# Kernel optimization log

Hardware: AMD Instinct MI355X
Metric: run time of the kernel (lower is better)

## Reference

```python
import jax, jax.numpy as jnp
import numpy as np

N_NODES, N_EDGES, D_IN, D_OUT = 50000, 800000, 64, 64
N_REL, N_TIME = 500, 1000


def setup_inputs() -> dict:
    key = jax.random.key(0)
    ks = jax.random.split(key, 14)
    xavier = lambda k, shape: jax.random.normal(k, shape, jnp.float32) * np.sqrt(2.0 / (shape[0] + shape[1])) * np.sqrt(2.0)
    return {
        "x": jax.random.normal(ks[0], (N_NODES, D_IN), jnp.float32),
        "rel_repr": jax.random.normal(ks[1], (N_REL, D_IN), jnp.float32),
        "time_emds": jax.random.normal(ks[2], (N_TIME, D_IN), jnp.float32),
        "src": jax.random.randint(ks[3], (N_EDGES,), 0, N_NODES),
        "dst": jax.random.randint(ks[4], (N_EDGES,), 0, N_NODES),
        "etype": jax.random.randint(ks[5], (N_EDGES,), 0, N_REL),
        "etime": jax.random.randint(ks[6], (N_EDGES,), 0, N_TIME),
        "trans_w": xavier(ks[7], (D_IN, D_OUT)),
        "loop_w": xavier(ks[8], (D_IN, D_OUT)),
        "w_rel": xavier(ks[9], (D_IN, D_OUT)),
        "attn_h": xavier(ks[10], (D_IN, 1)),
        "attn_t": xavier(ks[11], (D_IN, 1)),
        "attn_r": xavier(ks[12], (D_IN, 1)),
        "attn_ts": xavier(ks[13], (D_IN, 1)),
    }


def reference(x, rel_repr, time_emds, src, dst, etype, etime,
              trans_w, loop_w, w_rel, attn_h, attn_t, attn_r, attn_ts):
    n = x.shape[0]
    # per-node / per-rel / per-time scalar attention projections
    h_att = (x @ attn_h)[:, 0]          # [N]
    t_att = (x @ attn_t)[:, 0]          # [N]
    r_att = (rel_repr @ attn_r)[:, 0]   # [R]
    ts_att = (time_emds @ attn_ts)[:, 0]  # [T]
    # edge attention logits + edge_softmax grouped by destination node
    e = jax.nn.leaky_relu(h_att[src] - t_att[dst] + r_att[etype] + ts_att[etime], 0.1)  # [E]
    m = jax.ops.segment_max(e, dst, num_segments=n)
    ex = jnp.exp(e - m[dst])
    den = jax.ops.segment_sum(ex, dst, num_segments=n)
    att = (ex / den[dst])[:, None]      # [E,1]
    # message: (head + time) * (rel + time) -> trans_w -> weighted scatter-sum to dst
    time_emd = time_emds[etime]         # [E,D]
    edge_data = (x[src] + time_emd) * (rel_repr[etype] + time_emd)
    msg = (edge_data @ trans_w) * att   # [E,D_out]
    h = jax.ops.segment_sum(msg, dst, num_segments=n)
    x_out = h + x @ loop_w
    rel_out = rel_repr @ w_rel
    return (x_out, rel_out)
```

## Files before the change

kernel.cpp:

```cpp
#include <hip/hip_runtime.h>
#include <hip/hip_bf16.h>

#define N_NODES 50000
#define N_EDGES 800000
#define D 64
#define N_REL 500
#define N_TIME 1000
#define SLOTS 64
#define NODE_BLOCKS ((N_NODES + 63) / 64)
#define REL_BLOCKS  ((N_REL + 63) / 64)

__device__ __forceinline__ float bf2f(unsigned short u) {
    union { unsigned int i; float f; } v;
    v.i = ((unsigned int)u) << 16;
    return v.f;
}

__global__ void proj_kernel(const float* __restrict__ x,
                            const float* __restrict__ rel,
                            const float* __restrict__ tim,
                            const float* __restrict__ ah,
                            const float* __restrict__ at,
                            const float* __restrict__ ar,
                            const float* __restrict__ ats,
                            float* __restrict__ h_att, float* __restrict__ t_att,
                            float* __restrict__ r_att, float* __restrict__ ts_att,
                            unsigned short* __restrict__ x_bf) {
    int wave = (blockIdx.x * blockDim.x + threadIdx.x) >> 6;
    int lane = threadIdx.x & 63;
    const int total = N_NODES + N_REL + N_TIME;
    if (wave >= total) return;
    if (wave < N_NODES) {
        float xv = x[wave * D + lane];
        __hip_bfloat16 b = __float2bfloat16(xv);
        x_bf[wave * D + lane] = *(unsigned short*)&b;
        float s1 = xv * ah[lane];
        float s2 = xv * at[lane];
        for (int off = 32; off; off >>= 1) {
            s1 += __shfl_down(s1, off);
            s2 += __shfl_down(s2, off);
        }
        if (lane == 0) { h_att[wave] = s1; t_att[wave] = s2; }
    } else if (wave < N_NODES + N_REL) {
        int r = wave - N_NODES;
        float v = rel[r * D + lane] * ar[lane];
        for (int off = 32; off; off >>= 1) v += __shfl_down(v, off);
        if (lane == 0) r_att[r] = v;
    } else {
        int t = wave - N_NODES - N_REL;
        float v = tim[t * D + lane] * ats[lane];
        for (int off = 32; off; off >>= 1) v += __shfl_down(v, off);
        if (lane == 0) ts_att[t] = v;
    }
}

__global__ void build_kernel(const int* __restrict__ src, const int* __restrict__ dst,
                             const int* __restrict__ etype, const int* __restrict__ etime,
                             const float* __restrict__ h_att, const float* __restrict__ t_att,
                             const float* __restrict__ r_att, const float* __restrict__ ts_att,
                             int* __restrict__ cnt, int2* __restrict__ payload) {
    int i = blockIdx.x * blockDim.x + threadIdx.x;
    int e0 = i * 4;
    if (e0 >= N_EDGES) return;
    int4 s4 = *(const int4*)(src + e0);
    int4 d4 = *(const int4*)(dst + e0);
    int4 r4 = *(const int4*)(etype + e0);
    int4 t4 = *(const int4*)(etime + e0);
    int ss[4] = {s4.x, s4.y, s4.z, s4.w};
    int dd[4] = {d4.x, d4.y, d4.z, d4.w};
    int rr[4] = {r4.x, r4.y, r4.z, r4.w};
    int tt[4] = {t4.x, t4.y, t4.z, t4.w};
#pragma unroll
    for (int j = 0; j < 4; j++) {
        int s = ss[j], d = dd[j], r = rr[j], t = tt[j];
        float lg = h_att[s] - t_att[d] + r_att[r] + ts_att[t];
        float lr = lg > 0.f ? lg : 0.1f * lg;
        float ex = __expf(lr);
        unsigned exb = __float_as_uint(ex);
        int2 pl;
        pl.x = (int)((exb & ~7u) | (unsigned)(s & 7));
        pl.y = (int)(((unsigned)(s >> 3) << 19) | ((unsigned)r << 10) | (unsigned)t);
        int pos = atomicAdd(&cnt[d], 1);
        if (pos < SLOTS) payload[(d << 6) + pos] = pl;
    }
}

__global__ void node_gather_kernel(const unsigned short* __restrict__ x_bf,
                                   const float* __restrict__ rel,
                                   const float* __restrict__ tim,
                                   const int* __restrict__ cnt,
                                   const int2* __restrict__ payload,
                                   float* __restrict__ agg) {
    int d = (blockIdx.x * blockDim.x + threadIdx.x) >> 6;
    int lane = threadIdx.x & 63;
    if (d >= N_NODES) return;
    int deg = cnt[d];
    if (deg > SLOTS) deg = SLOTS;

    int s_l = 0, r_l = 0, t_l = 0;
    float ex = 0.f;
    if (lane < deg) {
        int2 pl = payload[(d << 6) + lane];
        unsigned px = (unsigned)pl.x;
        unsigned py = (unsigned)pl.y;
        ex = __uint_as_float(px & ~7u);
        s_l = (int)(((py >> 19) << 3) | (px & 7u));
        r_l = (int)((py >> 10) & 511u);
        t_l = (int)(py & 1023u);
    }
    float den = ex;
    for (int off = 32; off; off >>= 1) den += __shfl_xor(den, off);
    float att_l = (lane < deg) ? ex / den : 0.f;

    int qw = lane >> 4;
    int ql = lane & 15;
    float4 acc = make_float4(0.f, 0.f, 0.f, 0.f);
    for (int i = 0; i < deg; i += 4) {
        int ei = i + qw;
        int s = __shfl(s_l, ei);
        int r = __shfl(r_l, ei);
        int t = __shfl(t_l, ei);
        float att = __shfl(att_l, ei);
        float4  te = *(const float4*)(tim + t * D + ql * 4);
        ushort4 xb = *(const ushort4*)(x_bf + s * D + ql * 4);
        float4  rl = *(const float4*)(rel + r * D + ql * 4);
        acc.x += att * (bf2f(xb.x) + te.x) * (rl.x + te.x);
        acc.y += att * (bf2f(xb.y) + te.y) * (rl.y + te.y);
        acc.z += att * (bf2f(xb.z) + te.z) * (rl.z + te.z);
        acc.w += att * (bf2f(xb.w) + te.w) * (rl.w + te.w);
    }
    for (int off = 16; off <= 32; off <<= 1) {
        acc.x += __shfl_xor(acc.x, off);
        acc.y += __shfl_xor(acc.y, off);
        acc.z += __shfl_xor(acc.z, off);
        acc.w += __shfl_xor(acc.w, off);
    }
    if (qw == 0)
        *(float4*)(agg + (d << 7) + ql * 4) = acc;
}

__global__ __launch_bounds__(256, 4)
void out_gemm_kernel(const float* __restrict__ agg,
                     const float* __restrict__ x,
                     const float* __restrict__ rel,
                     const float* __restrict__ trans_w,
                     const float* __restrict__ loop_w,
                     const float* __restrict__ w_rel,
                     float* __restrict__ out) {
    __shared__ float Wa[D * D];
    __shared__ float Wb[D * D];
    int t = threadIdx.x;
    bool nodeb = blockIdx.x < NODE_BLOCKS;

    for (int j = 0; j < 4; j++) {
        int idx = (t + 256 * j) * 4;
        if (nodeb) {
            *(float4*)(Wa + idx) = *(const float4*)(trans_w + idx);
            *(float4*)(Wb + idx) = *(const float4*)(loop_w + idx);
        } else {
            *(float4*)(Wa + idx) = *(const float4*)(w_rel + idx);
        }
    }
    __syncthreads();

    int lane = t & 63;
    int wv = t >> 6;
    int c4 = (lane & 15) << 2;
    int r0 = wv * 16 + (lane >> 4) * 4;

    float acc[4][4];
    for (int i = 0; i < 4; i++)
        for (int c = 0; c < 4; c++) acc[i][c] = 0.f;

    if (nodeb) {
        int row0 = blockIdx.x * 64;
        for (int k = 0; k < D; k += 4) {
            float wt[4][4], wl[4][4];
            for (int kk = 0; kk < 4; kk++) {
                *(float4*)&wt[kk][0] = *(const float4*)(Wa + (k + kk) * D + c4);
                *(float4*)&wl[kk][0] = *(const float4*)(Wb + (k + kk) * D + c4);
            }
            for (int i = 0; i < 4; i++) {
                int gr = row0 + r0 + i;
                if (gr >= N_NODES) gr = N_NODES - 1;
                float a[4], xv[4];
                *(float4*)&a[0]  = *(const float4*)(agg + (size_t)gr * 128 + k);
                *(float4*)&xv[0] = *(const float4*)(x   + (size_t)gr * D + k);
                for (int c = 0; c < 4; c++) {
                    float s = acc[i][c];
                    for (int kk = 0; kk < 4; kk++)
                        s += a[kk] * wt[kk][c] + xv[kk] * wl[kk][c];
                    acc[i][c] = s;
                }
            }
        }
        for (int i = 0; i < 4; i++) {
            int gr = row0 + r0 + i;
            if (gr < N_NODES)
                *(float4*)(out + (size_t)gr * D + c4) = *(float4*)&acc[i][0];
        }
    } else {
        int row0 = (blockIdx.x - NODE_BLOCKS) * 64;
        for (int k = 0; k < D; k += 4) {
            float wt[4][4];
            for (int kk = 0; kk < 4; kk++)
                *(float4*)&wt[kk][0] = *(const float4*)(Wa + (k + kk) * D + c4);
            for (int i = 0; i < 4; i++) {
                int gr = row0 + r0 + i;
                if (gr >= N_REL) gr = N_REL - 1;
                float a[4];
                *(float4*)&a[0] = *(const float4*)(rel + (size_t)gr * D + k);
                for (int c = 0; c < 4; c++) {
                    float s = acc[i][c];
                    for (int kk = 0; kk < 4; kk++)
                        s += a[kk] * wt[kk][c];
                    acc[i][c] = s;
                }
            }
        }
        for (int i = 0; i < 4; i++) {
            int gr = row0 + r0 + i;
            if (gr < N_REL)
                *(float4*)(out + (size_t)(N_NODES + gr) * D + c4) = *(float4*)&acc[i][0];
        }
    }
}

extern "C" void kernel_launch(void* const* d_in, const int* in_sizes, int n_in,
                              void* d_out, int out_size, void* d_ws, size_t ws_size,
                              hipStream_t stream) {
    const float* x    = (const float*)d_in[0];
    const float* rel  = (const float*)d_in[1];
    const float* tim  = (const float*)d_in[2];
    const int* src   = (const int*)d_in[3];
    const int* dst   = (const int*)d_in[4];
    const int* etype = (const int*)d_in[5];
    const int* etime = (const int*)d_in[6];
    const float* trans_w = (const float*)d_in[7];
    const float* loop_w  = (const float*)d_in[8];
    const float* w_rel   = (const float*)d_in[9];
    const float* ah  = (const float*)d_in[10];
    const float* at  = (const float*)d_in[11];
    const float* ar  = (const float*)d_in[12];
    const float* ats = (const float*)d_in[13];

    char* ws = (char*)d_ws;
    int*   cnt            = (int*)  (ws);
    float* h_att          = (float*)(ws + 200000);
    float* t_att          = (float*)(ws + 400000);
    float* r_att          = (float*)(ws + 600000);
    float* ts_att         = (float*)(ws + 602000);
    int2*  payload        = (int2*) (ws + 1000000);
    float* agg            = (float*)(ws + 1000000);
    unsigned short* x_bf  = (unsigned short*)(ws + 26600000);

    float* out = (float*)d_out;

    hipMemsetAsync(cnt, 0, N_NODES * sizeof(int), stream);

    {
        int waves = N_NODES + N_REL + N_TIME;
        proj_kernel<<<(waves + 3) / 4, 256, 0, stream>>>(
            x, rel, tim, ah, at, ar, ats,
            h_att, t_att, r_att, ts_att, x_bf);
    }
    {
        int threads = N_EDGES / 4;
        build_kernel<<<(threads + 127) / 128, 128, 0, stream>>>(
            src, dst, etype, etime, h_att, t_att, r_att, ts_att, cnt, payload);
    }
    {
        node_gather_kernel<<<(N_NODES + 3) / 4, 256, 0, stream>>>(
            x_bf, rel, tim, cnt, payload, agg);
    }
    {
        out_gemm_kernel<<<NODE_BLOCKS + REL_BLOCKS, 256, 0, stream>>>(
            agg, x, rel, trans_w, loop_w, w_rel, out);
    }
}
```

Measured before the change: 206.1 us.

## Partition edge bucketing by destination range per XCD with persistent work stealing

Replaces the flat edge-bucketing kernel with a persistent kernel. Each block reads its hardware XCC id and works through destination-node ranges, starting with the one owned by its XCD, so each XCD's L2 holds only its own slice of the counter and payload arrays. Work comes from per-range atomic task counters. Each range first runs 250 tasks that read the payload slice into L2 as a prefetch, then scans edge chunks with nontemporal loads and skips chunks with no destinations in the range. In exchange, every XCD rereads the whole dst array eight times over, and the task atomics and barriers add overhead.

```diff
diff --git a/kernel.cpp b/kernel.cpp
--- a/kernel.cpp
+++ b/kernel.cpp
@@ -9,6 +9,16 @@
 #define SLOTS 64
 #define NODE_BLOCKS ((N_NODES + 63) / 64)
 #define REL_BLOCKS  ((N_REL + 63) / 64)
+
+#define N_XCD 8
+#define DST_PER_XCD (N_NODES / N_XCD)
+#define CHUNK 4096
+#define NCH ((N_EDGES + CHUNK - 1) / CHUNK)
+#define PRIME 250
+#define TASKS (PRIME + NCH)
+
+typedef int  vint4  __attribute__((ext_vector_type(4)));
+typedef float vflt4 __attribute__((ext_vector_type(4)));
 
 __device__ __forceinline__ float bf2f(unsigned short u) {
     union { unsigned int i; float f; } v;
@@ -54,35 +64,73 @@
     }
 }
 
-__global__ void build_kernel(const int* __restrict__ src, const int* __restrict__ dst,
-                             const int* __restrict__ etype, const int* __restrict__ etime,
-                             const float* __restrict__ h_att, const float* __restrict__ t_att,
-                             const float* __restrict__ r_att, const float* __restrict__ ts_att,
-                             int* __restrict__ cnt, int2* __restrict__ payload) {
-    int i = blockIdx.x * blockDim.x + threadIdx.x;
-    int e0 = i * 4;
-    if (e0 >= N_EDGES) return;
-    int4 s4 = *(const int4*)(src + e0);
-    int4 d4 = *(const int4*)(dst + e0);
-    int4 r4 = *(const int4*)(etype + e0);
-    int4 t4 = *(const int4*)(etime + e0);
-    int ss[4] = {s4.x, s4.y, s4.z, s4.w};
-    int dd[4] = {d4.x, d4.y, d4.z, d4.w};
-    int rr[4] = {r4.x, r4.y, r4.z, r4.w};
-    int tt[4] = {t4.x, t4.y, t4.z, t4.w};
+__global__ __launch_bounds__(256, 4)
+void build_xcd_kernel(const int* __restrict__ src, const int* __restrict__ dst,
+                      const int* __restrict__ etype, const int* __restrict__ etime,
+                      const float* __restrict__ h_att, const float* __restrict__ t_att,
+                      const float* __restrict__ r_att, const float* __restrict__ ts_att,
+                      int* __restrict__ cnt, int2* __restrict__ payload,
+                      int* __restrict__ xcd_ctr, float* __restrict__ sink) {
+    int xcc;
+    asm volatile("s_getreg_b32 %0, hwreg(HW_REG_XCC_ID)" : "=s"(xcc));
+    xcc &= 7;
+    __shared__ int task_s;
+    float facc = 0.f;
+
+    for (int pass = 0; pass < N_XCD; pass++) {
+        int kk = (xcc + pass) & 7;
+        int dlo = kk * DST_PER_XCD;
+        while (true) {
+            if (threadIdx.x == 0) task_s = atomicAdd(&xcd_ctr[kk], 1);
+            __syncthreads();
+            int task = task_s;
+            __syncthreads();
+            if (task >= TASKS) break;
+            if (task < PRIME) {
+                const vflt4* p = (const vflt4*)(payload + (size_t)dlo * SLOTS)
+                                  + (size_t)task * 800;
+                for (int i = threadIdx.x; i < 800; i += 256) {
+                    vflt4 v = p[i];
+                    facc += v.x + v.y + v.z + v.w;
+                }
+            } else {
+                int base = (task - PRIME) * CHUNK;
+                for (int g = 0; g < CHUNK / 1024; g++) {
+                    int e0 = base + (g * 256 + threadIdx.x) * 4;
+                    if (e0 >= N_EDGES) break;
+                    vint4 d4 = __builtin_nontemporal_load((const vint4*)(dst + e0));
+                    int dd[4] = {d4.x, d4.y, d4.z, d4.w};
+                    bool any = ((unsigned)(dd[0] - dlo) < DST_PER_XCD) |
+                               ((unsigned)(dd[1] - dlo) < DST_PER_XCD) |
+                               ((unsigned)(dd[2] - dlo) < DST_PER_XCD) |
+                               ((unsigned)(dd[3] - dlo) < DST_PER_XCD);
+                    if (!any) continue;
+                    vint4 s4 = __builtin_nontemporal_load((const vint4*)(src + e0));
+                    vint4 r4 = __builtin_nontemporal_load((const vint4*)(etype + e0));
+                    vint4 t4 = __builtin_nontemporal_load((const vint4*)(etime + e0));
+                    int ss[4] = {s4.x, s4.y, s4.z, s4.w};
+                    int rr[4] = {r4.x, r4.y, r4.z, r4.w};
+                    int tt[4] = {t4.x, t4.y, t4.z, t4.w};
 #pragma unroll
-    for (int j = 0; j < 4; j++) {
-        int s = ss[j], d = dd[j], r = rr[j], t = tt[j];
-        float lg = h_att[s] - t_att[d] + r_att[r] + ts_att[t];
-        float lr = lg > 0.f ? lg : 0.1f * lg;
-        float ex = __expf(lr);
-        unsigned exb = __float_as_uint(ex);
-        int2 pl;
-        pl.x = (int)((exb & ~7u) | (unsigned)(s & 7));
-        pl.y = (int)(((unsigned)(s >> 3) << 19) | ((unsigned)r << 10) | (unsigned)t);
-        int pos = atomicAdd(&cnt[d], 1);
-        if (pos < SLOTS) payload[(d << 6) + pos] = pl;
-    }
+                    for (int j = 0; j < 4; j++) {
+                        int d = dd[j];
+                        if ((unsigned)(d - dlo) >= DST_PER_XCD) continue;
+                        int s = ss[j], r = rr[j], t = tt[j];
+                        float lg = h_att[s] - t_att[d] + r_att[r] + ts_att[t];
+                        float lr = lg > 0.f ? lg : 0.1f * lg;
+                        float ex = __expf(lr);
+                        unsigned exb = __float_as_uint(ex);
+                        int2 pl;
+                        pl.x = (int)((exb & ~7u) | (unsigned)(s & 7));
+                        pl.y = (int)(((unsigned)(s >> 3) << 19) | ((unsigned)r << 10) | (unsigned)t);
+                        int pos = atomicAdd(&cnt[d], 1);
+                        if (pos < SLOTS) payload[(d << 6) + pos] = pl;
+                    }
+                }
+            }
+        }
+    }
+    if (facc == 1.2345e-38f) *sink = facc;
 }
 
 __global__ void node_gather_kernel(const unsigned short* __restrict__ x_bf,
@@ -246,17 +294,19 @@
 
     char* ws = (char*)d_ws;
     int*   cnt            = (int*)  (ws);
-    float* h_att          = (float*)(ws + 200000);
-    float* t_att          = (float*)(ws + 400000);
-    float* r_att          = (float*)(ws + 600000);
-    float* ts_att         = (float*)(ws + 602000);
+    int*   xcd_ctr        = (int*)  (ws + 200000);
+    float* h_att          = (float*)(ws + 200064);
+    float* t_att          = (float*)(ws + 400064);
+    float* r_att          = (float*)(ws + 600064);
+    float* ts_att         = (float*)(ws + 602064);
+    float* sink           = (float*)(ws + 606080);
     int2*  payload        = (int2*) (ws + 1000000);
     float* agg            = (float*)(ws + 1000000);
     unsigned short* x_bf  = (unsigned short*)(ws + 26600000);
 
     float* out = (float*)d_out;
 
-    hipMemsetAsync(cnt, 0, N_NODES * sizeof(int), stream);
+    (void)hipMemsetAsync(ws, 0, 200064, stream);
 
     {
         int waves = N_NODES + N_REL + N_TIME;
@@ -265,9 +315,9 @@
             h_att, t_att, r_att, ts_att, x_bf);
     }
     {
-        int threads = N_EDGES / 4;
-        build_kernel<<<(threads + 127) / 128, 128, 0, stream>>>(
-            src, dst, etype, etime, h_att, t_att, r_att, ts_att, cnt, payload);
+        build_xcd_kernel<<<2048, 256, 0, stream>>>(
+            src, dst, etype, etime, h_att, t_att, r_att, ts_att,
+            cnt, payload, xcd_ctr, sink);
     }
     {
         node_gather_kernel<<<(N_NODES + 3) / 4, 256, 0, stream>>>(
```

New measurement: 411.3 us. +99.5%, slower.
